# Kernel tuning notes

Measured on AMD Instinct MI355X. Metric: run time of the kernel, lower is better.

## Reference

```python
import jax, jax.numpy as jnp
import numpy as np

N_NODES = 100000
N_EDGES = 1600000
D = 128


def setup_inputs() -> dict:
    key = jax.random.key(0)
    k0, k1, k2, k3 = jax.random.split(key, 4)
    x = jax.random.normal(k0, (N_NODES, D), dtype=jnp.float32)
    edge_index = jax.random.randint(k1, (2, N_EDGES), 0, N_NODES, dtype=jnp.int32)
    # Glorot-ish init for GCNConv weights; zero bias (PyG default)
    W1 = jax.random.normal(k2, (D, D), dtype=jnp.float32) / np.sqrt(D).astype(np.float32)
    b1 = jnp.zeros((D,), dtype=jnp.float32)
    W2 = jax.random.normal(k3, (D, D), dtype=jnp.float32) / np.sqrt(D).astype(np.float32)
    b2 = jnp.zeros((D,), dtype=jnp.float32)
    return {"x": x, "edge_index": edge_index, "W1": W1, "b1": b1, "W2": W2, "b2": b2}


def _gcn_layer(x, src, dst, norm, W, b, n_nodes):
    # PyG GCNConv: linear transform first, then normalized aggregation over A+I.
    h = x @ W                                    # [N, D_out]
    coef = norm[src] * norm[dst]                 # [E] symmetric normalization
    msgs = h[src] * coef[:, None]                # [E, D_out] gathered edge messages
    agg = jax.ops.segment_sum(msgs, dst, num_segments=n_nodes)
    agg = agg + h * (norm * norm)[:, None]       # self-loop contribution deg^{-1} * h
    return agg + b


def reference(x, edge_index, W1, b1, W2, b2):
    n_nodes = x.shape[0]
    src, dst = edge_index[0], edge_index[1]
    # degree of A + I (self-loops added), computed on destination nodes
    deg = jax.ops.segment_sum(jnp.ones(src.shape[0], dtype=x.dtype), dst,
                              num_segments=n_nodes) + 1.0
    norm = jax.lax.rsqrt(deg)                    # deg^{-1/2}
    # Layer 1: GCNConv -> ReLU (dropout is identity in eval mode)
    h = jax.nn.relu(_gcn_layer(x, src, dst, norm, W1, b1, n_nodes))
    # Layer 2
    h = jax.nn.relu(_gcn_layer(h, src, dst, norm, W2, b2, n_nodes))
    return h
```

## Files before the change

kernel.cpp:

```cpp
#include <hip/hip_runtime.h>

#define D 128
#define EG 4096
#define PADW 8

typedef _Float16 h8 __attribute__((ext_vector_type(8)));
typedef _Float16 h2 __attribute__((ext_vector_type(2)));
typedef float f4 __attribute__((ext_vector_type(4)));
typedef unsigned u4 __attribute__((ext_vector_type(4)));


__global__ __launch_bounds__(256) void hist_k(const int* __restrict__ dst,
                                              int* __restrict__ counts,
                                              int E, int NB, int G) {
  __shared__ int hist[512];
  int g = blockIdx.x, t = threadIdx.x;
  for (int b = t; b < NB; b += 256) hist[b] = 0;
  __syncthreads();
  int e0 = g * EG;
#pragma unroll
  for (int it = 0; it < EG / 256; ++it) {
    int e = e0 + it * 256 + t;
    if (e < E) atomicAdd(&hist[dst[e] >> 8], 1);
  }
  __syncthreads();
  for (int b = t; b < NB; b += 256) counts[b * G + g] = hist[b];
}

__global__ __launch_bounds__(256) void bsum_k(const int* __restrict__ in,
                                              int* __restrict__ bsum, int M) {
  __shared__ int s[256];
  int t = threadIdx.x, i = blockIdx.x * 256 + t;
  s[t] = (i < M) ? in[i] : 0;
  __syncthreads();
  for (int off = 128; off > 0; off >>= 1) {
    if (t < off) s[t] += s[t + off];
    __syncthreads();
  }
  if (t == 0) bsum[blockIdx.x] = s[0];
}

__global__ __launch_bounds__(1024) void bscan_k(int* bsum, int nb) {
  __shared__ int s[1024];
  int t = threadIdx.x;
  s[t] = (t < nb) ? bsum[t] : 0;
  __syncthreads();
  for (int off = 1; off < 1024; off <<= 1) {
    int v = (t >= off) ? s[t - off] : 0;
    __syncthreads();
    s[t] += v;
    __syncthreads();
  }
  if (t < nb) bsum[t] = s[t];
}

__global__ __launch_bounds__(256) void scanfin_k(const int* __restrict__ in,
                                                 const int* __restrict__ bsum_incl,
                                                 int* __restrict__ outx, int M) {
  __shared__ int s[256];
  int b = blockIdx.x, t = threadIdx.x, i = b * 256 + t;
  int v0 = (i < M) ? in[i] : 0;
  s[t] = v0;
  __syncthreads();
  for (int off = 1; off < 256; off <<= 1) {
    int v = (t >= off) ? s[t - off] : 0;
    __syncthreads();
    s[t] += v;
    __syncthreads();
  }
  int base = (b > 0) ? bsum_incl[b - 1] : 0;
  if (i < M) outx[i] = base + s[t] - v0;
}

__global__ __launch_bounds__(256) void scatter_k(const int* __restrict__ src,
                                                 const int* __restrict__ dst,
                                                 const int* __restrict__ cscan,
                                                 unsigned* __restrict__ tmp,
                                                 int E, int NB, int G) {
  __shared__ int hist[512];
  __shared__ int base[512];
  int g = blockIdx.x, t = threadIdx.x;
  for (int b = t; b < NB; b += 256) {
    hist[b] = 0;
    base[b] = cscan[b * G + g];
  }
  __syncthreads();
  int e0 = g * EG;
#pragma unroll
  for (int it = 0; it < EG / 256; ++it) {
    int e = e0 + it * 256 + t;
    if (e < E) {
      int d = dst[e];
      int b = d >> 8;
      int r = atomicAdd(&hist[b], 1);
      tmp[base[b] + r] = ((unsigned)(d & 255) << 20) | (unsigned)src[e];
    }
  }
}

__global__ __launch_bounds__(256) void bucket_k(const unsigned* __restrict__ tmp,
                                                const int* __restrict__ cscan,
                                                float* __restrict__ nrm,
                                                int2* __restrict__ rs2,
                                                int* __restrict__ eoff,
                                                int N, int E, int NB, int G) {
  __shared__ int cnt[256];
  __shared__ int sc[256];
  __shared__ int cur[256];
  int b = blockIdx.x, t = threadIdx.x;
  int seg0 = cscan[b * G];
  int seg1 = (b == NB - 1) ? E : cscan[(b + 1) * G];
  int pbase = seg0 + b * 256 * (PADW - 1);
  cnt[t] = 0;
  __syncthreads();
  for (int i = seg0 + t; i < seg1; i += 256)
    atomicAdd(&cnt[tmp[i] >> 20], 1);
  __syncthreads();
  int v0 = cnt[t];
  int pd = (v0 + PADW - 1) & ~(PADW - 1);
  sc[t] = pd;
  __syncthreads();
  for (int off = 1; off < 256; off <<= 1) {
    int v = (t >= off) ? sc[t - off] : 0;
    __syncthreads();
    sc[t] += v;
    __syncthreads();
  }
  int ex = sc[t] - pd;
  cur[t] = pbase + ex;
  int node = b * 256 + t;
  if (node < N) {
    rs2[node] = make_int2(pbase + ex, pbase + ex + pd);
    nrm[node] = rsqrtf((float)v0 + 1.0f);
  }
  int dummy = N * 256;
  for (int k = v0; k < pd; ++k) eoff[pbase + ex + k] = dummy;
  __syncthreads();
  for (int i = seg0 + t; i < seg1; i += 256) {
    unsigned p = tmp[i];
    int r = atomicAdd(&cur[p >> 20], 1);
    eoff[r] = (int)((p & 0xFFFFF) << 8);
  }
}

__global__ void zero_k(_Float16* __restrict__ Hh, int N) {
  int t = threadIdx.x;
  if (t < 128) Hh[(size_t)N * D + t] = (_Float16)0.f;
}

__global__ __launch_bounds__(256) void wtrans_k(const float* __restrict__ W,
                                                _Float16* __restrict__ WT) {
  int idx = blockIdx.x * 256 + threadIdx.x;
  int k = idx >> 7, col = idx & 127;
  WT[col * D + k] = (_Float16)W[idx];
}

template <bool FP32IN>
__global__ __launch_bounds__(256) void gemm_k(const void* __restrict__ Xv,
                                              const _Float16* __restrict__ WT,
                                              const float* __restrict__ nrm,
                                              _Float16* __restrict__ Hh, int N) {
  __shared__ _Float16 Wl[D * 136];
  int tid = threadIdx.x;
#pragma unroll
  for (int it = 0; it < 8; ++it) {
    int idx = it * 256 + tid;
    int col = idx >> 4, kseg = idx & 15;
    *(h8*)&Wl[col * 136 + kseg * 8] = *(const h8*)&WT[col * D + kseg * 8];
  }
  __syncthreads();
  int wave = tid >> 6, lane = tid & 63;
  int lr = lane & 15, lk = lane >> 4;
#pragma unroll
  for (int tt = 0; tt < 2; ++tt) {
    int tile = blockIdx.x * 8 + wave * 2 + tt;
    int row0 = tile * 16;
    if (row0 >= N) break;
    int row = row0 + lr;
    int rowc = row < N ? row : N - 1;
    h8 a[4];
    if constexpr (FP32IN) {
      const float* X = (const float*)Xv;
#pragma unroll
      for (int ks = 0; ks < 4; ++ks) {
        f4 p = *(const f4*)&X[(size_t)rowc * D + ks * 32 + lk * 8];
        f4 q = *(const f4*)&X[(size_t)rowc * D + ks * 32 + lk * 8 + 4];
        h8 t;
        t[0] = (_Float16)p[0]; t[1] = (_Float16)p[1];
        t[2] = (_Float16)p[2]; t[3] = (_Float16)p[3];
        t[4] = (_Float16)q[0]; t[5] = (_Float16)q[1];
        t[6] = (_Float16)q[2]; t[7] = (_Float16)q[3];
        a[ks] = t;
      }
    } else {
      const _Float16* X = (const _Float16*)Xv;
#pragma unroll
      for (int ks = 0; ks < 4; ++ks)
        a[ks] = *(const h8*)&X[(size_t)rowc * D + ks * 32 + lk * 8];
    }
    f4 acc[8];
#pragma unroll
    for (int ct = 0; ct < 8; ++ct) acc[ct] = (f4){0.f, 0.f, 0.f, 0.f};
#pragma unroll
    for (int ct = 0; ct < 8; ++ct) {
#pragma unroll
      for (int ks = 0; ks < 4; ++ks) {
        h8 b = *(const h8*)&Wl[(ct * 16 + lr) * 136 + ks * 32 + lk * 8];
        acc[ct] = __builtin_amdgcn_mfma_f32_16x16x32_f16(a[ks], b, acc[ct], 0, 0, 0);
      }
    }
#pragma unroll
    for (int r = 0; r < 4; ++r) {
      int ro = row0 + lk * 4 + r;
      if (ro < N) {
        float sc = nrm[ro];
#pragma unroll
        for (int ct = 0; ct < 8; ++ct)
          Hh[(size_t)ro * D + ct * 16 + lr] = (_Float16)(acc[ct][r] * sc);
      }
    }
  }
}

template <bool F16OUT>
__global__ __launch_bounds__(256) void agg_k(const _Float16* __restrict__ Hh,
                                             const float* __restrict__ nrm,
                                             const int2* __restrict__ rs2,
                                             const int* __restrict__ eoff,
                                             const float* __restrict__ bias,
                                             void* __restrict__ outv, int N) {
  int wave = threadIdx.x >> 6, lane = threadIdx.x & 63;
  int n = blockIdx.x * 4 + wave;
  if (n >= N) return;
  int grp = lane >> 4, sub = lane & 15;
  unsigned soff = (unsigned)sub * 16u;
  int2 se = rs2[n];
  const char* base = (const char*)Hh;
  const h2 ones = {(_Float16)1.f, (_Float16)1.f};
  float acc[8] = {};
  for (int i = se.x; i < se.y; i += PADW) {
    int e0 = i + grp * 2;
    unsigned o0 = (unsigned)eoff[e0] + soff;
    unsigned o1 = (unsigned)eoff[e0 + 1] + soff;
    u4 v0 = *(const u4*)(base + o0);
    u4 v1 = *(const u4*)(base + o1);
#pragma unroll
    for (int k = 0; k < 4; ++k) {
      unsigned lo = __builtin_amdgcn_perm(v1[k], v0[k], 0x05040100u);
      unsigned hi = __builtin_amdgcn_perm(v1[k], v0[k], 0x07060302u);
      acc[2 * k] = __builtin_amdgcn_fdot2(__builtin_bit_cast(h2, lo), ones,
                                          acc[2 * k], false);
      acc[2 * k + 1] = __builtin_amdgcn_fdot2(__builtin_bit_cast(h2, hi), ones,
                                              acc[2 * k + 1], false);
    }
  }
#pragma unroll
  for (int j = 0; j < 8; ++j) acc[j] += __shfl_xor(acc[j], 16);
#pragma unroll
  for (int j = 0; j < 8; ++j) acc[j] += __shfl_xor(acc[j], 32);
  if (grp == 0) {
    int d0 = sub * 8;
    h8 hv = *(const h8*)&Hh[(size_t)n * D + d0];
    float nn = nrm[n];
    f4 bl = *(const f4*)&bias[d0];
    f4 bh = *(const f4*)&bias[d0 + 4];
    float o[8];
#pragma unroll
    for (int j = 0; j < 8; ++j) {
      float bj = (j < 4) ? bl[j] : bh[j - 4];
      o[j] = fmaxf((acc[j] + (float)hv[j]) * nn + bj, 0.f);
    }
    if constexpr (F16OUT) {
      _Float16* out = (_Float16*)outv;
      h8 ov;
#pragma unroll
      for (int j = 0; j < 8; ++j) ov[j] = (_Float16)o[j];
      *(h8*)&out[(size_t)n * D + d0] = ov;
    } else {
      float* out = (float*)outv;
      f4 lo = {o[0], o[1], o[2], o[3]};
      f4 hi = {o[4], o[5], o[6], o[7]};
      *(f4*)&out[(size_t)n * D + d0] = lo;
      *(f4*)&out[(size_t)n * D + d0 + 4] = hi;
    }
  }
}


extern "C" void kernel_launch(void* const* d_in, const int* in_sizes, int n_in,
                              void* d_out, int out_size, void* d_ws, size_t ws_size,
                              hipStream_t stream) {
  const float* x  = (const float*)d_in[0];
  const int*   ei = (const int*)d_in[1];
  const float* W1 = (const float*)d_in[2];
  const float* b1 = (const float*)d_in[3];
  const float* W2 = (const float*)d_in[4];
  const float* b2 = (const float*)d_in[5];
  float* out = (float*)d_out;

  int N = in_sizes[0] / D;
  int E = in_sizes[1] / 2;
  const int* srcp = ei;
  const int* dstp = ei + E;

  int NB = (N + 255) / 256;
  int G  = (E + EG - 1) / EG;
  int M  = NB * G;
  int nbM = (M + 255) / 256;

  char* ws = (char*)d_ws;
  size_t off = 0;
  auto alloc = [&](size_t bytes) -> char* {
    char* p = ws + off;
    off = (off + bytes + 511) & ~(size_t)511;
    return p;
  };
  _Float16* Hh   = (_Float16*)alloc((size_t)(N + 1) * D * 2);
  _Float16* O1h  = (_Float16*)alloc((size_t)N * D * 2);
  float* normv     = (float*)alloc((size_t)N * 4);
  int2*  rs2       = (int2*)alloc((size_t)N * 8);
  int*   counts    = (int*)alloc((size_t)M * 4);
  int*   cscan     = (int*)alloc((size_t)M * 4);
  unsigned* tmp    = (unsigned*)alloc((size_t)E * 4);
  int*   eoff      = (int*)alloc((size_t)(E + NB * 256 * (PADW - 1)) * 4);
  int*   bsum      = (int*)alloc(4096);
  _Float16* WT1    = (_Float16*)alloc((size_t)D * D * 2);
  _Float16* WT2    = (_Float16*)alloc((size_t)D * D * 2);

  int tiles = (N + 15) / 16;
  int nbGemm = (tiles + 7) / 8;
  int nbAgg = (N + 3) / 4;

  wtrans_k<<<64, 256, 0, stream>>>(W1, WT1);
  wtrans_k<<<64, 256, 0, stream>>>(W2, WT2);
  zero_k<<<1, 128, 0, stream>>>(Hh, N);

  hist_k<<<G, 256, 0, stream>>>(dstp, counts, E, NB, G);
  bsum_k<<<nbM, 256, 0, stream>>>(counts, bsum, M);
  bscan_k<<<1, 1024, 0, stream>>>(bsum, nbM);
  scanfin_k<<<nbM, 256, 0, stream>>>(counts, bsum, cscan, M);
  scatter_k<<<G, 256, 0, stream>>>(srcp, dstp, cscan, tmp, E, NB, G);
  bucket_k<<<NB, 256, 0, stream>>>(tmp, cscan, normv, rs2, eoff, N, E, NB, G);

  gemm_k<true><<<nbGemm, 256, 0, stream>>>(x, WT1, normv, Hh, N);
  agg_k<true><<<nbAgg, 256, 0, stream>>>(Hh, normv, rs2, eoff, b1, O1h, N);
  gemm_k<false><<<nbGemm, 256, 0, stream>>>(O1h, WT2, normv, Hh, N);
  agg_k<false><<<nbAgg, 256, 0, stream>>>(Hh, normv, rs2, eoff, b2, out, N);
}
```

Before: 220.9 us.

## Split aggregation by feature slice across blocks and fold self-loop into edge list

The aggregation kernel now assigns 8 threads per node, each handling 4 bytes of a 32-byte feature slice. Eight blocks cover the 128 features for 32 nodes, so each block's gathers touch a narrower, more cache-friendly slice of H. The self-loop is inserted as an explicit first entry of each node's padded edge list, which removes the separate epilogue read of the node's own row. Edge offsets are prefetched one iteration ahead with nontemporal loads, and outputs are written with nontemporal stores. The cost is eight times more blocks, each re-reading rs2 and the offset list, plus slightly longer padded segments.

New measurement: 496.2 us. +124.6%, slower.

```diff
diff --git a/kernel.cpp b/kernel.cpp
--- a/kernel.cpp
+++ b/kernel.cpp
@@ -7,6 +7,7 @@
 typedef _Float16 h8 __attribute__((ext_vector_type(8)));
 typedef _Float16 h2 __attribute__((ext_vector_type(2)));
 typedef float f4 __attribute__((ext_vector_type(4)));
+typedef float f2 __attribute__((ext_vector_type(2)));
 typedef unsigned u4 __attribute__((ext_vector_type(4)));
 
 
@@ -110,14 +111,15 @@
   int b = blockIdx.x, t = threadIdx.x;
   int seg0 = cscan[b * G];
   int seg1 = (b == NB - 1) ? E : cscan[(b + 1) * G];
-  int pbase = seg0 + b * 256 * (PADW - 1);
+  int pbase = (seg0 + b * 2056 + 7) & ~7;
   cnt[t] = 0;
   __syncthreads();
   for (int i = seg0 + t; i < seg1; i += 256)
     atomicAdd(&cnt[tmp[i] >> 20], 1);
   __syncthreads();
+  int node = b * 256 + t;
   int v0 = cnt[t];
-  int pd = (v0 + PADW - 1) & ~(PADW - 1);
+  int pd = (node < N) ? ((v0 + 1 + PADW - 1) & ~(PADW - 1)) : 0;
   sc[t] = pd;
   __syncthreads();
   for (int off = 1; off < 256; off <<= 1) {
@@ -127,14 +129,15 @@
     __syncthreads();
   }
   int ex = sc[t] - pd;
-  cur[t] = pbase + ex;
-  int node = b * 256 + t;
+  int rbeg = pbase + ex;
+  cur[t] = rbeg + 1;
   if (node < N) {
-    rs2[node] = make_int2(pbase + ex, pbase + ex + pd);
+    rs2[node] = make_int2(rbeg, rbeg + pd);
     nrm[node] = rsqrtf((float)v0 + 1.0f);
-  }
-  int dummy = N * 256;
-  for (int k = v0; k < pd; ++k) eoff[pbase + ex + k] = dummy;
+    eoff[rbeg] = node * 256;
+    int dummy = N * 256;
+    for (int k = v0 + 1; k < pd; ++k) eoff[rbeg + k] = dummy;
+  }
   __syncthreads();
   for (int i = seg0 + t; i < seg1; i += 256) {
     unsigned p = tmp[i];
@@ -229,60 +232,68 @@
                                              const int* __restrict__ eoff,
                                              const float* __restrict__ bias,
                                              void* __restrict__ outv, int N) {
-  int wave = threadIdx.x >> 6, lane = threadIdx.x & 63;
-  int n = blockIdx.x * 4 + wave;
+  int s = blockIdx.x & 7;
+  int c = blockIdx.x >> 3;
+  int grp = threadIdx.x >> 3;
+  int j = threadIdx.x & 7;
+  int n = c * 32 + grp;
   if (n >= N) return;
-  int grp = lane >> 4, sub = lane & 15;
-  unsigned soff = (unsigned)sub * 16u;
+  unsigned loff = (unsigned)(s * 32 + j * 4);
   int2 se = rs2[n];
   const char* base = (const char*)Hh;
   const h2 ones = {(_Float16)1.f, (_Float16)1.f};
-  float acc[8] = {};
-  for (int i = se.x; i < se.y; i += PADW) {
-    int e0 = i + grp * 2;
-    unsigned o0 = (unsigned)eoff[e0] + soff;
-    unsigned o1 = (unsigned)eoff[e0 + 1] + soff;
-    u4 v0 = *(const u4*)(base + o0);
-    u4 v1 = *(const u4*)(base + o1);
-#pragma unroll
-    for (int k = 0; k < 4; ++k) {
-      unsigned lo = __builtin_amdgcn_perm(v1[k], v0[k], 0x05040100u);
-      unsigned hi = __builtin_amdgcn_perm(v1[k], v0[k], 0x07060302u);
-      acc[2 * k] = __builtin_amdgcn_fdot2(__builtin_bit_cast(h2, lo), ones,
-                                          acc[2 * k], false);
-      acc[2 * k + 1] = __builtin_amdgcn_fdot2(__builtin_bit_cast(h2, hi), ones,
-                                              acc[2 * k + 1], false);
-    }
-  }
-#pragma unroll
-  for (int j = 0; j < 8; ++j) acc[j] += __shfl_xor(acc[j], 16);
-#pragma unroll
-  for (int j = 0; j < 8; ++j) acc[j] += __shfl_xor(acc[j], 32);
-  if (grp == 0) {
-    int d0 = sub * 8;
-    h8 hv = *(const h8*)&Hh[(size_t)n * D + d0];
-    float nn = nrm[n];
-    f4 bl = *(const f4*)&bias[d0];
-    f4 bh = *(const f4*)&bias[d0 + 4];
-    float o[8];
-#pragma unroll
-    for (int j = 0; j < 8; ++j) {
-      float bj = (j < 4) ? bl[j] : bh[j - 4];
-      o[j] = fmaxf((acc[j] + (float)hv[j]) * nn + bj, 0.f);
-    }
-    if constexpr (F16OUT) {
-      _Float16* out = (_Float16*)outv;
-      h8 ov;
-#pragma unroll
-      for (int j = 0; j < 8; ++j) ov[j] = (_Float16)o[j];
-      *(h8*)&out[(size_t)n * D + d0] = ov;
-    } else {
-      float* out = (float*)outv;
-      f4 lo = {o[0], o[1], o[2], o[3]};
-      f4 hi = {o[4], o[5], o[6], o[7]};
-      *(f4*)&out[(size_t)n * D + d0] = lo;
-      *(f4*)&out[(size_t)n * D + d0 + 4] = hi;
-    }
+  float a0 = 0.f, a1 = 0.f;
+  int i = se.x;
+  u4 o0 = __builtin_nontemporal_load((const u4*)&eoff[i]);
+  u4 o1 = __builtin_nontemporal_load((const u4*)&eoff[i + 4]);
+  while (true) {
+    unsigned w0 = *(const unsigned*)(base + o0[0] + loff);
+    unsigned w1 = *(const unsigned*)(base + o0[1] + loff);
+    unsigned w2 = *(const unsigned*)(base + o0[2] + loff);
+    unsigned w3 = *(const unsigned*)(base + o0[3] + loff);
+    unsigned w4 = *(const unsigned*)(base + o1[0] + loff);
+    unsigned w5 = *(const unsigned*)(base + o1[1] + loff);
+    unsigned w6 = *(const unsigned*)(base + o1[2] + loff);
+    unsigned w7 = *(const unsigned*)(base + o1[3] + loff);
+    i += PADW;
+    bool more = i < se.y;
+    if (more) {
+      o0 = __builtin_nontemporal_load((const u4*)&eoff[i]);
+      o1 = __builtin_nontemporal_load((const u4*)&eoff[i + 4]);
+    }
+    unsigned lo, hi;
+    lo = __builtin_amdgcn_perm(w1, w0, 0x05040100u);
+    hi = __builtin_amdgcn_perm(w1, w0, 0x07060302u);
+    a0 = __builtin_amdgcn_fdot2(__builtin_bit_cast(h2, lo), ones, a0, false);
+    a1 = __builtin_amdgcn_fdot2(__builtin_bit_cast(h2, hi), ones, a1, false);
+    lo = __builtin_amdgcn_perm(w3, w2, 0x05040100u);
+    hi = __builtin_amdgcn_perm(w3, w2, 0x07060302u);
+    a0 = __builtin_amdgcn_fdot2(__builtin_bit_cast(h2, lo), ones, a0, false);
+    a1 = __builtin_amdgcn_fdot2(__builtin_bit_cast(h2, hi), ones, a1, false);
+    lo = __builtin_amdgcn_perm(w5, w4, 0x05040100u);
+    hi = __builtin_amdgcn_perm(w5, w4, 0x07060302u);
+    a0 = __builtin_amdgcn_fdot2(__builtin_bit_cast(h2, lo), ones, a0, false);
+    a1 = __builtin_amdgcn_fdot2(__builtin_bit_cast(h2, hi), ones, a1, false);
+    lo = __builtin_amdgcn_perm(w7, w6, 0x05040100u);
+    hi = __builtin_amdgcn_perm(w7, w6, 0x07060302u);
+    a0 = __builtin_amdgcn_fdot2(__builtin_bit_cast(h2, lo), ones, a0, false);
+    a1 = __builtin_amdgcn_fdot2(__builtin_bit_cast(h2, hi), ones, a1, false);
+    if (!more) break;
+  }
+  float nn = nrm[n];
+  f2 bv = *(const f2*)&bias[s * 16 + j * 2];
+  float q0 = fmaxf(a0 * nn + bv[0], 0.f);
+  float q1 = fmaxf(a1 * nn + bv[1], 0.f);
+  if constexpr (F16OUT) {
+    h2 ov;
+    ov[0] = (_Float16)q0;
+    ov[1] = (_Float16)q1;
+    __builtin_nontemporal_store(__builtin_bit_cast(unsigned, ov),
+                                (unsigned*)((char*)outv + (size_t)n * 256 + loff));
+  } else {
+    f2 ov = {q0, q1};
+    __builtin_nontemporal_store(ov,
+                                (f2*)((char*)outv + (size_t)n * 512 + 2 * loff));
   }
 }
 
@@ -322,14 +333,14 @@
   int*   counts    = (int*)alloc((size_t)M * 4);
   int*   cscan     = (int*)alloc((size_t)M * 4);
   unsigned* tmp    = (unsigned*)alloc((size_t)E * 4);
-  int*   eoff      = (int*)alloc((size_t)(E + NB * 256 * (PADW - 1)) * 4);
+  int*   eoff      = (int*)alloc((size_t)(E + (size_t)NB * 2056 + 64) * 4);
   int*   bsum      = (int*)alloc(4096);
   _Float16* WT1    = (_Float16*)alloc((size_t)D * D * 2);
   _Float16* WT2    = (_Float16*)alloc((size_t)D * D * 2);
 
   int tiles = (N + 15) / 16;
   int nbGemm = (tiles + 7) / 8;
-  int nbAgg = (N + 3) / 4;
+  int nbAgg = 8 * ((N + 31) / 32);
 
   wtrans_k<<<64, 256, 0, stream>>>(W1, WT1);
   wtrans_k<<<64, 256, 0, stream>>>(W2, WT2);
```
